# Kernel optimization log

Hardware: AMD Instinct MI355X
Metric: run time of the kernel (lower is better)

## Reference

```python
import jax, jax.numpy as jnp
import numpy as np

B, N, T, F_IN = 4, 1024, 16, 32
H1, H2 = 128, 128
LH = H2 // 2          # LSTM hidden = 64
MLP_H = H2 // 4       # 32
NEG = -9e15
ALPHA = 0.2           # LeakyReLU slope


def _xavier(k, shape):
    lim = float(np.sqrt(6.0 / (shape[0] + shape[1])))
    return jax.random.uniform(k, shape, jnp.float32, -lim, lim)


def _unif(k, shape, s):
    return jax.random.uniform(k, shape, jnp.float32, -s, s)


def setup_inputs() -> dict:
    key = jax.random.key(0)
    ks = jax.random.split(key, 16)
    x = jax.random.normal(ks[0], (B, N, T, F_IN), dtype=jnp.float32)
    adj = jax.random.randint(ks[1], (B, N, N), 0, 2, dtype=jnp.int32)
    # GAT layer 1 & 2
    W1 = _xavier(ks[2], (F_IN, H1)); a1 = _xavier(ks[3], (2 * H1, 1))
    W2 = _xavier(ks[4], (H1, H2));   a2 = _xavier(ks[5], (2 * H2, 1))
    # LSTM (torch gate order i,f,g,o)
    s = 1.0 / np.sqrt(LH)
    W_ih = _unif(ks[6], (4 * LH, H2), s)
    W_hh = _unif(ks[7], (4 * LH, LH), s)
    b_ih = _unif(ks[8], (4 * LH,), s)
    b_hh = _unif(ks[9], (4 * LH,), s)
    # Output MLP: 64 -> 32 -> 1
    s1 = 1.0 / np.sqrt(LH)
    Wo1 = _unif(ks[10], (LH, MLP_H), s1); bo1 = _unif(ks[11], (MLP_H,), s1)
    s2 = 1.0 / np.sqrt(MLP_H)
    Wo2 = _unif(ks[12], (MLP_H, 1), s2);  bo2 = _unif(ks[13], (1,), s2)
    return {"x": x, "adj": adj, "W1": W1, "a1": a1, "W2": W2, "a2": a2,
            "W_ih": W_ih, "W_hh": W_hh, "b_ih": b_ih, "b_hh": b_hh,
            "Wo1": Wo1, "bo1": bo1, "Wo2": Wo2, "bo2": bo2}


def _gat(h, mask, W, a):
    # h: (B,N,Fin) -> (B,N,Fout). Decompose cat([Wh_i,Wh_j]) @ a into two rank-1 scores.
    Wh = h @ W                             # (B,N,Fout)
    Fo = W.shape[1]
    s_src = Wh @ a[:Fo, 0]                 # (B,N)
    s_dst = Wh @ a[Fo:, 0]                 # (B,N)
    e = jax.nn.leaky_relu(s_src[:, :, None] + s_dst[:, None, :], ALPHA)  # (B,N,N)
    att = jnp.where(mask, e, NEG)
    att = jax.nn.softmax(att, axis=-1)
    return jax.nn.elu(att @ Wh)            # GAT layer's own ELU (concat=True)


def reference(x, adj, W1, a1, W2, a2, W_ih, W_hh, b_ih, b_hh, Wo1, bo1, Wo2, bo2):
    mask = adj > 0                         # (B,N,N)

    def per_t(ht):                         # ht: (B,N,F_IN)
        h = jax.nn.elu(_gat(ht, mask, W1, a1))   # outer F.elu as in GNNModel.forward
        h = jax.nn.elu(_gat(h, mask, W2, a2))
        return h

    g = jax.vmap(per_t, in_axes=2, out_axes=2)(x)   # (B,N,T,H2)
    seq = g.reshape(B * N, T, H2)

    def step(carry, xt):
        h, c = carry
        gates = xt @ W_ih.T + b_ih + h @ W_hh.T + b_hh
        i, f, gg, o = jnp.split(gates, 4, axis=-1)
        c = jax.nn.sigmoid(f) * c + jax.nn.sigmoid(i) * jnp.tanh(gg)
        h = jax.nn.sigmoid(o) * jnp.tanh(c)
        return (h, c), None

    init = (jnp.zeros((B * N, LH), x.dtype), jnp.zeros((B * N, LH), x.dtype))
    (hT, _), _ = jax.lax.scan(step, init, jnp.swapaxes(seq, 0, 1))  # scan over T

    out = jax.nn.relu(hT @ Wo1 + bo1) @ Wo2 + bo2   # (B*N, 1)
    return out.reshape(B, N, 1)
```

## Files before the change

kernel.cpp:

```cpp
#include <hip/hip_runtime.h>
#include <hip/hip_bf16.h>
#include <math.h>

#define BB 4
#define NN 1024
#define TT 16
#define FIN 32
#define HH 128
#define LH 64
#define MLPH 32

typedef __attribute__((ext_vector_type(8))) short short8;
typedef __attribute__((ext_vector_type(4))) float f32x4;
typedef unsigned short u16;
typedef unsigned int u32;

union AFu { u32 u[4]; short8 s; };

__device__ __forceinline__ u16 f2b(float f) {
    union { float f; u32 u; } v; v.f = f;
    u32 u = v.u;
    return (u16)((u + 0x7FFFu + ((u >> 16) & 1u)) >> 16);
}
__device__ __forceinline__ float b2f(u16 h) {
    union { u32 u; float f; } v; v.u = ((u32)h) << 16;
    return v.f;
}
__device__ __forceinline__ float frcp(float x) {
    float r; asm("v_rcp_f32 %0, %1" : "=v"(r) : "v"(x)); return r;
}
__device__ __forceinline__ float fsig(float x) {
    return frcp(1.f + __expf(-x));
}
__device__ __forceinline__ float ftanh(float x) {
    return __builtin_fmaf(2.f, frcp(1.f + __expf(-2.f * x)), -1.f);
}
__device__ __forceinline__ void gload_lds16(const void* g, void* l) {
    __builtin_amdgcn_global_load_lds((const __attribute__((address_space(1))) unsigned int*)g,
                                     (__attribute__((address_space(3))) unsigned int*)l, 16, 0, 0);
}

__global__ __launch_bounds__(256) void k_pre(const float* __restrict__ W1, const float* __restrict__ W2,
                      const float* __restrict__ W_ih, const float* __restrict__ W_hh,
                      const float* __restrict__ b_ih, const float* __restrict__ b_hh,
                      u16* W1T, u16* W2T, u16* WihB, u16* WhhB, float* bsum) {
    int gi = blockIdx.x * 256 + threadIdx.x;
    for (int i = gi; i < 128 * 32; i += 16384) { int c = i >> 5, k = i & 31; W1T[i] = f2b(W1[k * 128 + c]); }
    for (int i = gi; i < 128 * 128; i += 16384) { int c = i >> 7, k = i & 127; W2T[i] = f2b(W2[k * 128 + c]); }
    for (int i = gi; i < 256 * 128; i += 16384) WihB[i] = f2b(W_ih[i]);
    for (int i = gi; i < 256 * 64; i += 16384) WhhB[i] = f2b(W_hh[i]);
    if (gi < 256) bsum[gi] = b_ih[gi] + b_hh[gi];
}

__global__ __launch_bounds__(256) void k_mask(const int* __restrict__ adj, u32* __restrict__ bmT) {
    int gw = (blockIdx.x * 256 + threadIdx.x) >> 6;
    int lane = threadIdx.x & 63;
    int base = gw << 4;
#pragma unroll 4
    for (int it = 0; it < 16; ++it) {
        int u = base + it;
        unsigned long long m = __ballot(adj[((size_t)u << 6) + lane] > 0);
        if (lane == 0) {
            int g = u & 15;
            int bi = u >> 4;
            int b = bi >> 10, i = bi & 1023;
            bmT[(((b << 5) + 2 * g) << 10) + i]     = (u32)m;
            bmT[(((b << 5) + 2 * g + 1) << 10) + i] = (u32)(m >> 32);
        }
    }
}


__global__ __launch_bounds__(256) void k_projA(const float* __restrict__ x, const u16* __restrict__ W1T,
                                               const float* __restrict__ a1,
                                               u16* __restrict__ WhT, float* __restrict__ ssrc,
                                               float* __restrict__ sdst) {
    __shared__ float tile[64][132];
    __shared__ float sA[256];
    int bt = blockIdx.x >> 4, i0 = (blockIdx.x & 15) << 6;
    int b = bt >> 4, t = bt & 15;
    int tid = threadIdx.x, w = tid >> 6, l = tid & 63;
    int lr = l & 15, lg = l >> 4;
    sA[tid] = a1[tid];
    int i = i0 + 16 * w + lr;
    const float* xp = x + ((size_t)((b << 10) + i) * TT + t) * FIN + 8 * lg;
    float4 x0 = *(const float4*)xp;
    float4 x1 = *(const float4*)(xp + 4);
    short8 af;
    af[0] = (short)f2b(x0.x); af[1] = (short)f2b(x0.y); af[2] = (short)f2b(x0.z); af[3] = (short)f2b(x0.w);
    af[4] = (short)f2b(x1.x); af[5] = (short)f2b(x1.y); af[6] = (short)f2b(x1.z); af[7] = (short)f2b(x1.w);
    f32x4 zz = {0.f, 0.f, 0.f, 0.f};
#pragma unroll
    for (int tc = 0; tc < 8; ++tc) {
        short8 bf = *(const short8*)(W1T + ((16 * tc + lr) << 5) + 8 * lg);
        f32x4 d = __builtin_amdgcn_mfma_f32_16x16x32_bf16(af, bf, zz, 0, 0, 0);
#pragma unroll
        for (int r = 0; r < 4; ++r) tile[16 * w + 4 * lg + r][16 * tc + lr] = d[r];
    }
    __syncthreads();
    if (tid < 128) {
        int r = tid & 63;
        const float* av = sA + ((tid < 64) ? 0 : 128);
        float s = 0.f;
#pragma unroll 4
        for (int c = 0; c < 128; ++c) s += tile[r][c] * av[c];
        ((tid < 64) ? ssrc : sdst)[(bt << 10) + i0 + r] = s;
    }
    {
        int c = tid & 127, hh2 = tid >> 7;
        u16 tmp[32];
#pragma unroll
        for (int j = 0; j < 32; ++j) tmp[j] = f2b(tile[32 * hh2 + j][c]);
        int tc = c >> 4, lr2 = c & 15;
        u16* dst = WhT + (size_t)bt * 131072 + ((i0 >> 5) + hh2) * 4096 + tc * 512 + lr2 * 8;
#pragma unroll
        for (int lg2 = 0; lg2 < 4; ++lg2) *(short8*)(dst + lg2 * 128) = *(const short8*)(tmp + 8 * lg2);
    }
}

__global__ __launch_bounds__(256) void k_projB(const u16* __restrict__ h1, const u16* __restrict__ W2T,
                                               const float* __restrict__ a2,
                                               u16* __restrict__ WhT, float* __restrict__ ssrc,
                                               float* __restrict__ sdst) {
    __shared__ float tile[64][132];
    __shared__ float sA[256];
    int bt = blockIdx.x >> 4, i0 = (blockIdx.x & 15) << 6;
    int tid = threadIdx.x, w = tid >> 6, l = tid & 63;
    int lr = l & 15, lg = l >> 4;
    sA[tid] = a2[tid];
    const u16* ap = h1 + (size_t)bt * 131072 + ((i0 >> 4) + w) * 2048 + l * 8;
    f32x4 acc[8];
#pragma unroll
    for (int tc = 0; tc < 8; ++tc) acc[tc] = (f32x4){0.f, 0.f, 0.f, 0.f};
#pragma unroll
    for (int ch = 0; ch < 4; ++ch) {
        short8 af = *(const short8*)(ap + ch * 512);
#pragma unroll
        for (int tc = 0; tc < 8; ++tc) {
            short8 bf = *(const short8*)(W2T + ((16 * tc + lr) << 7) + 32 * ch + 8 * lg);
            acc[tc] = __builtin_amdgcn_mfma_f32_16x16x32_bf16(af, bf, acc[tc], 0, 0, 0);
        }
    }
#pragma unroll
    for (int tc = 0; tc < 8; ++tc)
#pragma unroll
        for (int r = 0; r < 4; ++r) tile[16 * w + 4 * lg + r][16 * tc + lr] = acc[tc][r];
    __syncthreads();
    if (tid < 128) {
        int r = tid & 63;
        const float* av = sA + ((tid < 64) ? 0 : 128);
        float s = 0.f;
#pragma unroll 4
        for (int c = 0; c < 128; ++c) s += tile[r][c] * av[c];
        ((tid < 64) ? ssrc : sdst)[(bt << 10) + i0 + r] = s;
    }
    {
        int c = tid & 127, hh2 = tid >> 7;
        u16 tmp[32];
#pragma unroll
        for (int j = 0; j < 32; ++j) tmp[j] = f2b(tile[32 * hh2 + j][c]);
        int tc = c >> 4, lr2 = c & 15;
        u16* dst = WhT + (size_t)bt * 131072 + ((i0 >> 5) + hh2) * 4096 + tc * 512 + lr2 * 8;
#pragma unroll
        for (int lg2 = 0; lg2 < 4; ++lg2) *(short8*)(dst + lg2 * 128) = *(const short8*)(tmp + 8 * lg2);
    }
}

#define ATTN_PROLOGUE                                                                \
    __shared__ __align__(16) u16 Bbuf[2][8192];                                      \
    __shared__ __align__(16) float Ej[1024];                                         \
    __shared__ __align__(16) float Fj[1024];                                         \
    int bt = blockIdx.x >> 2, i0b = (blockIdx.x & 3) << 8;                           \
    int b = bt >> 4;                                                                 \
    int tid = threadIdx.x, wv = tid >> 6, l = tid & 63;                              \
    int lr = l & 15, lg = l >> 4;                                                    \
    const u16* wbase = WhT + (size_t)bt * 131072;                                    \
    gload_lds16(wbase + (wv << 10) + l * 8,       &Bbuf[0][(wv << 10)]);             \
    gload_lds16(wbase + (wv << 10) + 512 + l * 8, &Bbuf[0][(wv << 10) + 512]);       \
    for (int k = tid; k < 1024; k += 512) {                                          \
        float sdv = sdst[(bt << 10) + k];                                            \
        Ej[k] = __expf(sdv);                                                         \
        Fj[k] = __expf(0.2f * sdv);                                                  \
    }                                                                                \
    int rb = i0b + (wv << 5);                                                        \
    const u32* mbase = bmT + ((size_t)b << 15);                                      \
    u32 mw0 = mbase[rb + lr];                                                        \
    u32 mw1 = mbase[rb + 16 + lr];                                                   \
    u32 mw2 = mbase[1024 + rb + lr];                                                 \
    u32 mw3 = mbase[1024 + rb + 16 + lr];                                            \
    float si0 = ssrc[(bt << 10) + rb + lr];                                          \
    float si1 = ssrc[(bt << 10) + rb + 16 + lr];                                     \
    float Ei0 = __expf(si0), Fi0 = __expf(0.2f * si0);                               \
    float Ei1 = __expf(si1), Fi1 = __expf(0.2f * si1);                               \
    f32x4 acc[2][8];                                                                 \
    _Pragma("unroll")                                                                \
    for (int rt = 0; rt < 2; ++rt)                                                   \
        _Pragma("unroll")                                                            \
        for (int tc = 0; tc < 8; ++tc) acc[rt][tc] = (f32x4){0.f, 0.f, 0.f, 0.f};    \
    f32x4 accd[2];                                                                   \
    accd[0] = (f32x4){0.f, 0.f, 0.f, 0.f};                                           \
    accd[1] = (f32x4){0.f, 0.f, 0.f, 0.f};                                           \
    short8 bone;                                                                     \
    _Pragma("unroll")                                                                \
    for (int e = 0; e < 8; ++e) bone[e] = (short)0x3F80;                             \
    __syncthreads();

#define PHALF(AF, EI, FI, WW)                                                        \
    {                                                                                \
        u32 byt = ((WW) >> (lg << 3)) & 0xFFu;                                       \
        float pA[8] = {fmaxf((EI) * e0.x, (FI) * f0.x), fmaxf((EI) * e0.y, (FI) * f0.y), \
                       fmaxf((EI) * e0.z, (FI) * f0.z), fmaxf((EI) * e0.w, (FI) * f0.w), \
                       fmaxf((EI) * e1.x, (FI) * f1.x), fmaxf((EI) * e1.y, (FI) * f1.y), \
                       fmaxf((EI) * e1.z, (FI) * f1.z), fmaxf((EI) * e1.w, (FI) * f1.w)}; \
        _Pragma("unroll")                                                            \
        for (int q = 0; q < 4; ++q) {                                                \
            u32 m0 = (u32)(-(int)((byt >> (2 * q)) & 1u));                           \
            u32 m1 = (u32)(-(int)((byt >> (2 * q + 1)) & 1u));                       \
            float p0 = __uint_as_float(__float_as_uint(pA[2 * q]) & m0);             \
            float p1 = __uint_as_float(__float_as_uint(pA[2 * q + 1]) & m1);         \
            asm("v_cvt_pk_bf16_f32 %0, %1, %2" : "=v"(AF.u[q]) : "v"(p0), "v"(p1));  \
        }                                                                            \
    }

#define COMPUTE(JC, CUR, JCL, W0, W1)                                                \
    {                                                                                \
        const float* ejp = Ej + ((JC) << 5) + (lg << 3);                             \
        const float* fjp = Fj + ((JC) << 5) + (lg << 3);                             \
        float4 e0 = *(const float4*)ejp, e1 = *(const float4*)(ejp + 4);             \
        float4 f0 = *(const float4*)fjp, f1 = *(const float4*)(fjp + 4);             \
        AFu af0, af1;                                                                \
        PHALF(af0, Ei0, Fi0, W0)                                                     \
        PHALF(af1, Ei1, Fi1, W1)                                                     \
        _Pragma("unroll")                                                            \
        for (int tc = 0; tc < 8; ++tc) {                                             \
            short8 bfr = *(const short8*)(&Bbuf[CUR][(JCL) * 4096 + tc * 512 + l * 8]); \
            acc[0][tc] = __builtin_amdgcn_mfma_f32_16x16x32_bf16(af0.s, bfr, acc[0][tc], 0, 0, 0); \
            acc[1][tc] = __builtin_amdgcn_mfma_f32_16x16x32_bf16(af1.s, bfr, acc[1][tc], 0, 0, 0); \
        }                                                                            \
        accd[0] = __builtin_amdgcn_mfma_f32_16x16x32_bf16(af0.s, bone, accd[0], 0, 0, 0); \
        accd[1] = __builtin_amdgcn_mfma_f32_16x16x32_bf16(af1.s, bone, accd[1], 0, 0, 0); \
    }

#define ATTN_MAIN_LOOP                                                               \
    for (int c = 0; c < 16; ++c) {                                                   \
        int cur = c & 1;                                                             \
        if (c < 15) {                                                                \
            gload_lds16(wbase + (c + 1) * 8192 + (wv << 10) + l * 8,       &Bbuf[cur ^ 1][(wv << 10)]);       \
            gload_lds16(wbase + (c + 1) * 8192 + (wv << 10) + 512 + l * 8, &Bbuf[cur ^ 1][(wv << 10) + 512]); \
        }                                                                            \
        u32 nw0 = 0, nw1 = 0, nw2 = 0, nw3 = 0;                                      \
        if (c < 15) {                                                                \
            const u32* mp = mbase + ((2 * c + 2) << 10);                             \
            nw0 = mp[rb + lr];        nw1 = mp[rb + 16 + lr];                        \
            nw2 = mp[1024 + rb + lr]; nw3 = mp[1024 + rb + 16 + lr];                 \
        }                                                                            \
        COMPUTE(2 * c,     cur, 0, mw0, mw1)                                         \
        COMPUTE(2 * c + 1, cur, 1, mw2, mw3)                                         \
        mw0 = nw0; mw1 = nw1; mw2 = nw2; mw3 = nw3;                                  \
        __syncthreads();                                                             \
    }

__global__ __launch_bounds__(512) void k_attnH(const u16* __restrict__ WhT, const float* __restrict__ ssrc,
                                               const float* __restrict__ sdst, const u32* __restrict__ bmT,
                                               u16* __restrict__ hout) {
    ATTN_PROLOGUE
    ATTN_MAIN_LOOP

    char* hb = (char*)(&Bbuf[0][0]) + ((wv & 3) << 13);
    for (int pass = 0; pass < 2; ++pass) {
        if ((wv >> 2) == pass) {
#pragma unroll
            for (int rt = 0; rt < 2; ++rt) {
                float inv[4];
#pragma unroll
                for (int r = 0; r < 4; ++r) inv[r] = 1.f / accd[rt][r];
#pragma unroll
                for (int tc = 0; tc < 8; ++tc)
#pragma unroll
                    for (int r = 0; r < 4; ++r) {
                        float v = acc[rt][tc][r] * inv[r];
                        v = v > 0.f ? v : (__expf(v) - 1.f);
                        v = v > 0.f ? v : (__expf(v) - 1.f);
                        int row = (rt << 4) + (lg << 2) + r;
                        int col = (tc << 4) + lr;
                        *(u16*)(hb + (row << 8) + ((col << 1) ^ ((row & 7) << 4))) = f2b(v);
                    }
            }
            asm volatile("s_waitcnt lgkmcnt(0)" ::: "memory");
            __builtin_amdgcn_sched_barrier(0);
            int rtile0 = rb >> 4;
            u16* dstb = hout + (size_t)bt * 131072;
#pragma unroll
            for (int rt = 0; rt < 2; ++rt)
#pragma unroll
                for (int ch = 0; ch < 4; ++ch) {
                    int row = (rt << 4) + lr;
                    int colb = (ch << 5) + (lg << 3);
                    short8 v = *(const short8*)(hb + (row << 8) + ((colb << 1) ^ ((row & 7) << 4)));
                    *(short8*)(dstb + (size_t)(rtile0 + rt) * 2048 + ch * 512 + l * 8) = v;
                }
        }
        __syncthreads();
    }
}

__global__ __launch_bounds__(512, 2) void k_attnG(const u16* __restrict__ WhT, const float* __restrict__ ssrc,
                                                  const float* __restrict__ sdst, const u32* __restrict__ bmT,
                                                  const u16* __restrict__ WihB, const float* __restrict__ bsum,
                                                  u16* __restrict__ Gx) {
    ATTN_PROLOGUE
    ATTN_MAIN_LOOP

    int t = bt & 15;
    char* hb = (char*)(&Bbuf[0][0]) + (wv << 12);

#define EPI_STORE(RT)                                                                 \
    {                                                                                 \
        float inv[4];                                                                 \
        _Pragma("unroll")                                                             \
        for (int r = 0; r < 4; ++r) inv[r] = 1.f / accd[RT][r];                       \
        _Pragma("unroll")                                                             \
        for (int tc = 0; tc < 8; ++tc)                                                \
            _Pragma("unroll")                                                         \
            for (int r = 0; r < 4; ++r) {                                             \
                float v = acc[RT][tc][r] * inv[r];                                    \
                v = v > 0.f ? v : (__expf(v) - 1.f);                                  \
                v = v > 0.f ? v : (__expf(v) - 1.f);                                  \
                int row = (lg << 2) + r;                                              \
                int col = (tc << 4) + lr;                                             \
                *(u16*)(hb + (row << 8) + ((col << 1) ^ ((row & 7) << 4))) = f2b(v);  \
            }                                                                         \
        asm volatile("s_waitcnt lgkmcnt(0)" ::: "memory");                            \
        __builtin_amdgcn_sched_barrier(0);                                            \
    }

#define EPI_OUT_GX(RT)                                                                \
    {                                                                                 \
        int node = i0b + (wv << 5) + ((RT) << 4);                                     \
        int grpx = (b << 6) + (node >> 4);                                            \
        u16* gdst = Gx + (size_t)t * 1048576 + (size_t)grpx * 4096 + l * 8;           \
        _Pragma("unroll")                                                             \
        for (int half = 0; half < 2; ++half) {                                        \
            f32x4 accg[8];                                                            \
            _Pragma("unroll")                                                         \
            for (int tq = 0; tq < 8; ++tq) accg[tq] = (f32x4){0.f, 0.f, 0.f, 0.f};    \
            _Pragma("unroll")                                                         \
            for (int ch = 0; ch < 4; ++ch) {                                          \
                short8 af2 = *(const short8*)(hb + (lr << 8) + (((ch << 6) + (lg << 4)) ^ ((lr & 7) << 4))); \
                _Pragma("unroll")                                                     \
                for (int tq = 0; tq < 8; ++tq) {                                      \
                    int tc = (half << 3) + tq;                                        \
                    short8 bf = *(const short8*)(WihB + ((16 * tc + lr) << 7) + (ch << 5) + 8 * lg); \
                    accg[tq] = __builtin_amdgcn_mfma_f32_16x16x32_bf16(af2, bf, accg[tq], 0, 0, 0); \
                }                                                                     \
            }                                                                         \
            _Pragma("unroll")                                                         \
            for (int qq = 0; qq < 4; ++qq) {                                          \
                int tc0 = (half << 3) + 2 * qq;                                       \
                short8 v;                                                             \
                _Pragma("unroll")                                                     \
                for (int r = 0; r < 4; ++r) {                                         \
                    v[r]     = (short)f2b(accg[2 * qq][r]     + bsum[(tc0 << 4) + lr]); \
                    v[4 + r] = (short)f2b(accg[2 * qq + 1][r] + bsum[((tc0 + 1) << 4) + lr]); \
                }                                                                     \
                *(short8*)(gdst + ((half << 2) + qq) * 512) = v;                      \
            }                                                                         \
        }                                                                             \
    }

    EPI_STORE(0)
    EPI_OUT_GX(0)
    asm volatile("s_waitcnt lgkmcnt(0)" ::: "memory");
    __builtin_amdgcn_sched_barrier(0);
    EPI_STORE(1)
    EPI_OUT_GX(1)

#undef EPI_STORE
#undef EPI_OUT_GX
}

#undef ATTN_PROLOGUE
#undef ATTN_MAIN_LOOP
#undef PHALF
#undef COMPUTE

__global__ __launch_bounds__(256, 1) void k_lstm(const u16* __restrict__ Gx, const u16* __restrict__ WhhB,
                                                 const float* __restrict__ Wo1, const float* __restrict__ bo1,
                                                 const float* __restrict__ Wo2, const float* __restrict__ bo2,
                                                 float* __restrict__ out) {
    __shared__ u16 hls[16 * 72];
    __shared__ float hf[16 * 65];
    __shared__ float wo1[64 * 32];
    __shared__ float wo2[32];
    int grp = blockIdx.x;
    int m0 = grp << 4;
    int tid = threadIdx.x, wv = tid >> 6, l = tid & 63;
    int lr = l & 15, lg = l >> 4;
    for (int k = tid; k < 64 * 32; k += 256) wo1[k] = Wo1[k];
    if (tid < 32) wo2[tid] = Wo2[tid];
    for (int k = tid; k < 16 * 72; k += 256) hls[k] = 0;
    short8 bh[4][2];
#pragma unroll
    for (int tq = 0; tq < 4; ++tq)
#pragma unroll
        for (int ch = 0; ch < 2; ++ch)
            bh[tq][ch] = *(const short8*)(WhhB + ((16 * (wv + 4 * tq) + lr) << 6) + 32 * ch + 8 * lg);
    float cst[4], hreg[4];
#pragma unroll
    for (int r = 0; r < 4; ++r) { cst[r] = 0.f; hreg[r] = 0.f; }
    int sub = wv & 1;
    const u16* gp = Gx + ((size_t)grp << 12) + ((size_t)(wv >> 1) << 9) + l * 8;
    short8 gx0[4], gx1[4];
#pragma unroll
    for (int tq = 0; tq < 4; ++tq) gx0[tq] = *(const short8*)(gp + tq * 1024);
    __syncthreads();
#pragma unroll
    for (int t = 0; t < TT; ++t) {
        if (t < 15) {
#pragma unroll
            for (int tq = 0; tq < 4; ++tq) {
                short8 v = *(const short8*)(gp + (size_t)(t + 1) * 1048576 + tq * 1024);
                if (t & 1) gx0[tq] = v; else gx1[tq] = v;
            }
        }
        f32x4 acc[4];
#pragma unroll
        for (int tq = 0; tq < 4; ++tq) {
            short8 v = (t & 1) ? gx1[tq] : gx0[tq];
#pragma unroll
            for (int r = 0; r < 4; ++r)
                acc[tq][r] = b2f((u16)v[(sub << 2) + r]);
        }
#pragma unroll
        for (int ch = 0; ch < 2; ++ch) {
            short8 af = *(const short8*)(hls + lr * 72 + 32 * ch + 8 * lg);
#pragma unroll
            for (int tq = 0; tq < 4; ++tq)
                acc[tq] = __builtin_amdgcn_mfma_f32_16x16x32_bf16(af, bh[tq][ch], acc[tq], 0, 0, 0);
        }
#pragma unroll
        for (int r = 0; r < 4; ++r) {
            float iv = fsig(acc[0][r]);
            float fv = fsig(acc[1][r]);
            float gv = ftanh(acc[2][r]);
            float ov = fsig(acc[3][r]);
            float cn = __builtin_fmaf(fv, cst[r], iv * gv);
            cst[r] = cn;
            hreg[r] = ov * ftanh(cn);
        }
        __syncthreads();
#pragma unroll
        for (int r = 0; r < 4; ++r)
            hls[(4 * lg + r) * 72 + 16 * wv + lr] = f2b(hreg[r]);
        __syncthreads();
    }
#pragma unroll
    for (int r = 0; r < 4; ++r)
        hf[(4 * lg + r) * 65 + 16 * wv + lr] = hreg[r];
    __syncthreads();
    if (wv == 0) {
        int r = lr, p = lg;
        float hid[8];
#pragma unroll
        for (int q = 0; q < 8; ++q) hid[q] = bo1[8 * p + q];
        for (int j = 0; j < 64; ++j) {
            float hv = hf[r * 65 + j];
#pragma unroll
            for (int q = 0; q < 8; ++q) hid[q] += hv * wo1[j * 32 + 8 * p + q];
        }
        float po = 0.f;
#pragma unroll
        for (int q = 0; q < 8; ++q) po += fmaxf(hid[q], 0.f) * wo2[8 * p + q];
        po += __shfl_xor(po, 16);
        po += __shfl_xor(po, 32);
        if (p == 0) out[m0 + r] = po + bo2[0];
    }
}

extern "C" void kernel_launch(void* const* d_in, const int* in_sizes, int n_in,
                              void* d_out, int out_size, void* d_ws, size_t ws_size,
                              hipStream_t stream) {
    const float* x    = (const float*)d_in[0];
    const int*   adj  = (const int*)d_in[1];
    const float* W1   = (const float*)d_in[2];
    const float* a1   = (const float*)d_in[3];
    const float* W2   = (const float*)d_in[4];
    const float* a2   = (const float*)d_in[5];
    const float* W_ih = (const float*)d_in[6];
    const float* W_hh = (const float*)d_in[7];
    const float* b_ih = (const float*)d_in[8];
    const float* b_hh = (const float*)d_in[9];
    const float* Wo1  = (const float*)d_in[10];
    const float* bo1  = (const float*)d_in[11];
    const float* Wo2  = (const float*)d_in[12];
    const float* bo2  = (const float*)d_in[13];
    float* out = (float*)d_out;

    char* w = (char*)d_ws;
    const size_t SLOT = (size_t)8388608 * sizeof(u16);
    u16* A  = (u16*)w;
    u16* Bf = (u16*)(w + SLOT);
    u16* C  = (u16*)(w + 2 * SLOT);
    char* sm = w + 3 * SLOT;
    float* s1s = (float*)sm;
    float* s1d = s1s + 65536;
    float* s2s = s1d + 65536;
    float* s2d = s2s + 65536;
    u32* BM  = (u32*)(s2d + 65536);
    u16* W1T = (u16*)(BM + 131072);
    u16* W2T = W1T + 4096;
    u16* WihB = W2T + 16384;
    u16* WhhB = WihB + 32768;
    float* BS = (float*)(WhhB + 16384);
    u16* Gx = Bf;

    k_pre<<<64, 256, 0, stream>>>(W1, W2, W_ih, W_hh, b_ih, b_hh, W1T, W2T, WihB, WhhB, BS);
    k_mask<<<1024, 256, 0, stream>>>(adj, BM);
    k_projA<<<1024, 256, 0, stream>>>(x, W1T, a1, A, s1s, s1d);
    k_attnH<<<256, 512, 0, stream>>>(A, s1s, s1d, BM, Bf);
    k_projB<<<1024, 256, 0, stream>>>(Bf, W2T, a2, C, s2s, s2d);
    k_attnG<<<256, 512, 0, stream>>>(C, s2s, s2d, BM, WihB, BS, Gx);
    k_lstm<<<256, 256, 0, stream>>>(Gx, WhhB, Wo1, bo1, Wo2, bo2, out);
}
```

Baseline: 166.7 us.

## Fuse layer-2 GAT projection and score computation into layer-1 attention epilogue

Removes the separate k_projB kernel and performs the layer-2 W2 projection plus src/dst attention scores inside k_attnH's epilogue. Each wave writes its ELU'd tile to LDS, runs MFMA against W2T and stores the bf16 Wh2 tile directly, reducing the scores with shuffles. This drops a kernel launch and the global round-trip of the hidden activations, but adds register pressure (launch bounds now 512,2) and W2T global reads in every block.

```diff
diff --git a/kernel.cpp b/kernel.cpp
--- a/kernel.cpp
+++ b/kernel.cpp
@@ -11,6 +11,7 @@
 #define MLPH 32
 
 typedef __attribute__((ext_vector_type(8))) short short8;
+typedef __attribute__((ext_vector_type(4))) short short4v;
 typedef __attribute__((ext_vector_type(4))) float f32x4;
 typedef unsigned short u16;
 typedef unsigned int u32;
@@ -97,54 +98,6 @@
 #pragma unroll
         for (int r = 0; r < 4; ++r) tile[16 * w + 4 * lg + r][16 * tc + lr] = d[r];
     }
-    __syncthreads();
-    if (tid < 128) {
-        int r = tid & 63;
-        const float* av = sA + ((tid < 64) ? 0 : 128);
-        float s = 0.f;
-#pragma unroll 4
-        for (int c = 0; c < 128; ++c) s += tile[r][c] * av[c];
-        ((tid < 64) ? ssrc : sdst)[(bt << 10) + i0 + r] = s;
-    }
-    {
-        int c = tid & 127, hh2 = tid >> 7;
-        u16 tmp[32];
-#pragma unroll
-        for (int j = 0; j < 32; ++j) tmp[j] = f2b(tile[32 * hh2 + j][c]);
-        int tc = c >> 4, lr2 = c & 15;
-        u16* dst = WhT + (size_t)bt * 131072 + ((i0 >> 5) + hh2) * 4096 + tc * 512 + lr2 * 8;
-#pragma unroll
-        for (int lg2 = 0; lg2 < 4; ++lg2) *(short8*)(dst + lg2 * 128) = *(const short8*)(tmp + 8 * lg2);
-    }
-}
-
-__global__ __launch_bounds__(256) void k_projB(const u16* __restrict__ h1, const u16* __restrict__ W2T,
-                                               const float* __restrict__ a2,
-                                               u16* __restrict__ WhT, float* __restrict__ ssrc,
-                                               float* __restrict__ sdst) {
-    __shared__ float tile[64][132];
-    __shared__ float sA[256];
-    int bt = blockIdx.x >> 4, i0 = (blockIdx.x & 15) << 6;
-    int tid = threadIdx.x, w = tid >> 6, l = tid & 63;
-    int lr = l & 15, lg = l >> 4;
-    sA[tid] = a2[tid];
-    const u16* ap = h1 + (size_t)bt * 131072 + ((i0 >> 4) + w) * 2048 + l * 8;
-    f32x4 acc[8];
-#pragma unroll
-    for (int tc = 0; tc < 8; ++tc) acc[tc] = (f32x4){0.f, 0.f, 0.f, 0.f};
-#pragma unroll
-    for (int ch = 0; ch < 4; ++ch) {
-        short8 af = *(const short8*)(ap + ch * 512);
-#pragma unroll
-        for (int tc = 0; tc < 8; ++tc) {
-            short8 bf = *(const short8*)(W2T + ((16 * tc + lr) << 7) + 32 * ch + 8 * lg);
-            acc[tc] = __builtin_amdgcn_mfma_f32_16x16x32_bf16(af, bf, acc[tc], 0, 0, 0);
-        }
-    }
-#pragma unroll
-    for (int tc = 0; tc < 8; ++tc)
-#pragma unroll
-        for (int r = 0; r < 4; ++r) tile[16 * w + 4 * lg + r][16 * tc + lr] = acc[tc][r];
     __syncthreads();
     if (tid < 128) {
         int r = tid & 63;
@@ -260,48 +213,103 @@
         __syncthreads();                                                             \
     }
 
-__global__ __launch_bounds__(512) void k_attnH(const u16* __restrict__ WhT, const float* __restrict__ ssrc,
-                                               const float* __restrict__ sdst, const u32* __restrict__ bmT,
-                                               u16* __restrict__ hout) {
+__global__ __launch_bounds__(512, 2) void k_attnH(const u16* __restrict__ WhT, const float* __restrict__ ssrc,
+                                                  const float* __restrict__ sdst, const u32* __restrict__ bmT,
+                                                  const u16* __restrict__ W2T, const float* __restrict__ a2,
+                                                  u16* __restrict__ Wh2, float* __restrict__ s2s,
+                                                  float* __restrict__ s2d) {
     ATTN_PROLOGUE
     ATTN_MAIN_LOOP
 
-    char* hb = (char*)(&Bbuf[0][0]) + ((wv & 3) << 13);
-    for (int pass = 0; pass < 2; ++pass) {
-        if ((wv >> 2) == pass) {
-#pragma unroll
-            for (int rt = 0; rt < 2; ++rt) {
-                float inv[4];
-#pragma unroll
-                for (int r = 0; r < 4; ++r) inv[r] = 1.f / accd[rt][r];
-#pragma unroll
-                for (int tc = 0; tc < 8; ++tc)
-#pragma unroll
-                    for (int r = 0; r < 4; ++r) {
-                        float v = acc[rt][tc][r] * inv[r];
-                        v = v > 0.f ? v : (__expf(v) - 1.f);
-                        v = v > 0.f ? v : (__expf(v) - 1.f);
-                        int row = (rt << 4) + (lg << 2) + r;
-                        int col = (tc << 4) + lr;
-                        *(u16*)(hb + (row << 8) + ((col << 1) ^ ((row & 7) << 4))) = f2b(v);
-                    }
-            }
-            asm volatile("s_waitcnt lgkmcnt(0)" ::: "memory");
-            __builtin_amdgcn_sched_barrier(0);
-            int rtile0 = rb >> 4;
-            u16* dstb = hout + (size_t)bt * 131072;
-#pragma unroll
-            for (int rt = 0; rt < 2; ++rt)
-#pragma unroll
-                for (int ch = 0; ch < 4; ++ch) {
-                    int row = (rt << 4) + lr;
-                    int colb = (ch << 5) + (lg << 3);
-                    short8 v = *(const short8*)(hb + (row << 8) + ((colb << 1) ^ ((row & 7) << 4)));
-                    *(short8*)(dstb + (size_t)(rtile0 + rt) * 2048 + ch * 512 + l * 8) = v;
-                }
-        }
-        __syncthreads();
-    }
+    char* hb = (char*)(&Bbuf[0][0]) + (wv << 12);
+
+#define EPI_STORE(RT)                                                                 \
+    {                                                                                 \
+        float inv[4];                                                                 \
+        _Pragma("unroll")                                                             \
+        for (int r = 0; r < 4; ++r) inv[r] = 1.f / accd[RT][r];                       \
+        _Pragma("unroll")                                                             \
+        for (int tc = 0; tc < 8; ++tc)                                                \
+            _Pragma("unroll")                                                         \
+            for (int r = 0; r < 4; ++r) {                                             \
+                float v = acc[RT][tc][r] * inv[r];                                    \
+                v = v > 0.f ? v : (__expf(v) - 1.f);                                  \
+                v = v > 0.f ? v : (__expf(v) - 1.f);                                  \
+                int row = (lg << 2) + r;                                              \
+                int col = (tc << 4) + lr;                                             \
+                *(u16*)(hb + (row << 8) + ((col << 1) ^ ((row & 7) << 4))) = f2b(v);  \
+            }                                                                         \
+        asm volatile("s_waitcnt lgkmcnt(0)" ::: "memory");                            \
+        __builtin_amdgcn_sched_barrier(0);                                            \
+    }
+
+#define EPI_PROJB(RT)                                                                 \
+    {                                                                                 \
+        float ps[4], pd[4];                                                           \
+        _Pragma("unroll")                                                             \
+        for (int r = 0; r < 4; ++r) { ps[r] = 0.f; pd[r] = 0.f; }                     \
+        int grow = i0b + (wv << 5) + ((RT) << 4);                                     \
+        int jc = grow >> 5;                                                           \
+        u16* wout = Wh2 + (size_t)bt * 131072 + jc * 4096;                            \
+        int lg2 = 2 * (RT) + (lg >> 1);                                               \
+        _Pragma("unroll")                                                             \
+        for (int half = 0; half < 2; ++half) {                                        \
+            f32x4 accg[4];                                                            \
+            _Pragma("unroll")                                                         \
+            for (int tq = 0; tq < 4; ++tq) accg[tq] = (f32x4){0.f, 0.f, 0.f, 0.f};    \
+            _Pragma("unroll")                                                         \
+            for (int ch = 0; ch < 4; ++ch) {                                          \
+                short8 af2 = *(const short8*)(hb + (lr << 8) + (((ch << 6) + (lg << 4)) ^ ((lr & 7) << 4))); \
+                _Pragma("unroll")                                                     \
+                for (int tq = 0; tq < 4; ++tq) {                                      \
+                    int tc2 = (half << 2) + tq;                                       \
+                    short8 bf = *(const short8*)(W2T + ((16 * tc2 + lr) << 7) + (ch << 5) + 8 * lg); \
+                    accg[tq] = __builtin_amdgcn_mfma_f32_16x16x32_bf16(af2, bf, accg[tq], 0, 0, 0); \
+                }                                                                     \
+            }                                                                         \
+            _Pragma("unroll")                                                         \
+            for (int tq = 0; tq < 4; ++tq) {                                          \
+                int tc2 = (half << 2) + tq;                                           \
+                float a2sv = a2[16 * tc2 + lr];                                       \
+                float a2dv = a2[128 + 16 * tc2 + lr];                                 \
+                short4v w4;                                                           \
+                _Pragma("unroll")                                                     \
+                for (int r = 0; r < 4; ++r) {                                         \
+                    float wval = accg[tq][r];                                         \
+                    ps[r] = __builtin_fmaf(wval, a2sv, ps[r]);                        \
+                    pd[r] = __builtin_fmaf(wval, a2dv, pd[r]);                        \
+                    w4[r] = (short)f2b(wval);                                         \
+                }                                                                     \
+                *(short4v*)(wout + tc2 * 512 + lg2 * 128 + lr * 8 + (lg & 1) * 4) = w4; \
+            }                                                                         \
+        }                                                                             \
+        _Pragma("unroll")                                                             \
+        for (int r = 0; r < 4; ++r) {                                                 \
+            _Pragma("unroll")                                                         \
+            for (int o = 1; o < 16; o <<= 1) {                                        \
+                ps[r] += __shfl_xor(ps[r], o);                                        \
+                pd[r] += __shfl_xor(pd[r], o);                                        \
+            }                                                                         \
+        }                                                                             \
+        if (lr == 0) {                                                                \
+            _Pragma("unroll")                                                         \
+            for (int r = 0; r < 4; ++r) {                                             \
+                int row = grow + 4 * lg + r;                                          \
+                s2s[(bt << 10) + row] = ps[r];                                        \
+                s2d[(bt << 10) + row] = pd[r];                                        \
+            }                                                                         \
+        }                                                                             \
+    }
+
+    EPI_STORE(0)
+    EPI_PROJB(0)
+    asm volatile("s_waitcnt lgkmcnt(0)" ::: "memory");
+    __builtin_amdgcn_sched_barrier(0);
+    EPI_STORE(1)
+    EPI_PROJB(1)
+
+#undef EPI_STORE
+#undef EPI_PROJB
 }
 
 __global__ __launch_bounds__(512, 2) void k_attnG(const u16* __restrict__ WhT, const float* __restrict__ ssrc,
@@ -517,8 +525,7 @@
     k_pre<<<64, 256, 0, stream>>>(W1, W2, W_ih, W_hh, b_ih, b_hh, W1T, W2T, WihB, WhhB, BS);
     k_mask<<<1024, 256, 0, stream>>>(adj, BM);
     k_projA<<<1024, 256, 0, stream>>>(x, W1T, a1, A, s1s, s1d);
-    k_attnH<<<256, 512, 0, stream>>>(A, s1s, s1d, BM, Bf);
-    k_projB<<<1024, 256, 0, stream>>>(Bf, W2T, a2, C, s2s, s2d);
+    k_attnH<<<256, 512, 0, stream>>>(A, s1s, s1d, BM, W2T, a2, C, s2s, s2d);
     k_attnG<<<256, 512, 0, stream>>>(C, s2s, s2d, BM, WihB, BS, Gx);
     k_lstm<<<256, 256, 0, stream>>>(Gx, WhhB, Wo1, bo1, Wo2, bo2, out);
 }
```

After: 157.1 us. 1.06x faster.

## Fuse layer-2 projection into attention epilogue and use 1024-thread attention blocks

Applied to the files above, without the earlier changes.

The separate k_projB kernel is removed. Its bf16 MFMA projection by W2, along with the a2 source and destination score reductions, now runs in the k_attnH epilogue directly from a per-wave LDS tile, so layer-1 output no longer round-trips through global memory. Both attention kernels move from 512 to 1024 threads per block, with each wave owning 16 rows instead of 32. This halves per-wave accumulator registers but raises LDS use with a 64KB Hls buffer, and it forces one block per CU.

```diff
diff --git a/kernel.cpp b/kernel.cpp
--- a/kernel.cpp
+++ b/kernel.cpp
@@ -11,6 +11,7 @@
 #define MLPH 32
 
 typedef __attribute__((ext_vector_type(8))) short short8;
+typedef __attribute__((ext_vector_type(4))) short short4v;
 typedef __attribute__((ext_vector_type(4))) float f32x4;
 typedef unsigned short u16;
 typedef unsigned int u32;
@@ -118,100 +119,44 @@
     }
 }
 
-__global__ __launch_bounds__(256) void k_projB(const u16* __restrict__ h1, const u16* __restrict__ W2T,
-                                               const float* __restrict__ a2,
-                                               u16* __restrict__ WhT, float* __restrict__ ssrc,
-                                               float* __restrict__ sdst) {
-    __shared__ float tile[64][132];
-    __shared__ float sA[256];
-    int bt = blockIdx.x >> 4, i0 = (blockIdx.x & 15) << 6;
-    int tid = threadIdx.x, w = tid >> 6, l = tid & 63;
-    int lr = l & 15, lg = l >> 4;
-    sA[tid] = a2[tid];
-    const u16* ap = h1 + (size_t)bt * 131072 + ((i0 >> 4) + w) * 2048 + l * 8;
-    f32x4 acc[8];
-#pragma unroll
-    for (int tc = 0; tc < 8; ++tc) acc[tc] = (f32x4){0.f, 0.f, 0.f, 0.f};
-#pragma unroll
-    for (int ch = 0; ch < 4; ++ch) {
-        short8 af = *(const short8*)(ap + ch * 512);
-#pragma unroll
-        for (int tc = 0; tc < 8; ++tc) {
-            short8 bf = *(const short8*)(W2T + ((16 * tc + lr) << 7) + 32 * ch + 8 * lg);
-            acc[tc] = __builtin_amdgcn_mfma_f32_16x16x32_bf16(af, bf, acc[tc], 0, 0, 0);
-        }
-    }
-#pragma unroll
-    for (int tc = 0; tc < 8; ++tc)
-#pragma unroll
-        for (int r = 0; r < 4; ++r) tile[16 * w + 4 * lg + r][16 * tc + lr] = acc[tc][r];
-    __syncthreads();
-    if (tid < 128) {
-        int r = tid & 63;
-        const float* av = sA + ((tid < 64) ? 0 : 128);
-        float s = 0.f;
-#pragma unroll 4
-        for (int c = 0; c < 128; ++c) s += tile[r][c] * av[c];
-        ((tid < 64) ? ssrc : sdst)[(bt << 10) + i0 + r] = s;
-    }
-    {
-        int c = tid & 127, hh2 = tid >> 7;
-        u16 tmp[32];
-#pragma unroll
-        for (int j = 0; j < 32; ++j) tmp[j] = f2b(tile[32 * hh2 + j][c]);
-        int tc = c >> 4, lr2 = c & 15;
-        u16* dst = WhT + (size_t)bt * 131072 + ((i0 >> 5) + hh2) * 4096 + tc * 512 + lr2 * 8;
-#pragma unroll
-        for (int lg2 = 0; lg2 < 4; ++lg2) *(short8*)(dst + lg2 * 128) = *(const short8*)(tmp + 8 * lg2);
-    }
-}
-
 #define ATTN_PROLOGUE                                                                \
     __shared__ __align__(16) u16 Bbuf[2][8192];                                      \
     __shared__ __align__(16) float Ej[1024];                                         \
     __shared__ __align__(16) float Fj[1024];                                         \
+    __shared__ __align__(16) u16 Hls[16][2048];                                      \
     int bt = blockIdx.x >> 2, i0b = (blockIdx.x & 3) << 8;                           \
     int b = bt >> 4;                                                                 \
     int tid = threadIdx.x, wv = tid >> 6, l = tid & 63;                              \
     int lr = l & 15, lg = l >> 4;                                                    \
     const u16* wbase = WhT + (size_t)bt * 131072;                                    \
-    gload_lds16(wbase + (wv << 10) + l * 8,       &Bbuf[0][(wv << 10)]);             \
-    gload_lds16(wbase + (wv << 10) + 512 + l * 8, &Bbuf[0][(wv << 10) + 512]);       \
-    for (int k = tid; k < 1024; k += 512) {                                          \
-        float sdv = sdst[(bt << 10) + k];                                            \
-        Ej[k] = __expf(sdv);                                                         \
-        Fj[k] = __expf(0.2f * sdv);                                                  \
+    gload_lds16(wbase + (wv << 9) + l * 8, &Bbuf[0][(wv << 9)]);                     \
+    {                                                                                \
+        float sdv = sdst[(bt << 10) + tid];                                          \
+        Ej[tid] = __expf(sdv);                                                       \
+        Fj[tid] = __expf(0.2f * sdv);                                                \
     }                                                                                \
-    int rb = i0b + (wv << 5);                                                        \
+    int rb = i0b + (wv << 4);                                                        \
     const u32* mbase = bmT + ((size_t)b << 15);                                      \
     u32 mw0 = mbase[rb + lr];                                                        \
-    u32 mw1 = mbase[rb + 16 + lr];                                                   \
-    u32 mw2 = mbase[1024 + rb + lr];                                                 \
-    u32 mw3 = mbase[1024 + rb + 16 + lr];                                            \
+    u32 mw1 = mbase[1024 + rb + lr];                                                 \
     float si0 = ssrc[(bt << 10) + rb + lr];                                          \
-    float si1 = ssrc[(bt << 10) + rb + 16 + lr];                                     \
     float Ei0 = __expf(si0), Fi0 = __expf(0.2f * si0);                               \
-    float Ei1 = __expf(si1), Fi1 = __expf(0.2f * si1);                               \
-    f32x4 acc[2][8];                                                                 \
+    f32x4 acc[8];                                                                    \
     _Pragma("unroll")                                                                \
-    for (int rt = 0; rt < 2; ++rt)                                                   \
-        _Pragma("unroll")                                                            \
-        for (int tc = 0; tc < 8; ++tc) acc[rt][tc] = (f32x4){0.f, 0.f, 0.f, 0.f};    \
-    f32x4 accd[2];                                                                   \
-    accd[0] = (f32x4){0.f, 0.f, 0.f, 0.f};                                           \
-    accd[1] = (f32x4){0.f, 0.f, 0.f, 0.f};                                           \
+    for (int tc = 0; tc < 8; ++tc) acc[tc] = (f32x4){0.f, 0.f, 0.f, 0.f};            \
+    f32x4 accd = (f32x4){0.f, 0.f, 0.f, 0.f};                                        \
     short8 bone;                                                                     \
     _Pragma("unroll")                                                                \
     for (int e = 0; e < 8; ++e) bone[e] = (short)0x3F80;                             \
     __syncthreads();
 
-#define PHALF(AF, EI, FI, WW)                                                        \
+#define PHALF(AF, WW)                                                                \
     {                                                                                \
         u32 byt = ((WW) >> (lg << 3)) & 0xFFu;                                       \
-        float pA[8] = {fmaxf((EI) * e0.x, (FI) * f0.x), fmaxf((EI) * e0.y, (FI) * f0.y), \
-                       fmaxf((EI) * e0.z, (FI) * f0.z), fmaxf((EI) * e0.w, (FI) * f0.w), \
-                       fmaxf((EI) * e1.x, (FI) * f1.x), fmaxf((EI) * e1.y, (FI) * f1.y), \
-                       fmaxf((EI) * e1.z, (FI) * f1.z), fmaxf((EI) * e1.w, (FI) * f1.w)}; \
+        float pA[8] = {fmaxf(Ei0 * e0.x, Fi0 * f0.x), fmaxf(Ei0 * e0.y, Fi0 * f0.y), \
+                       fmaxf(Ei0 * e0.z, Fi0 * f0.z), fmaxf(Ei0 * e0.w, Fi0 * f0.w), \
+                       fmaxf(Ei0 * e1.x, Fi0 * f1.x), fmaxf(Ei0 * e1.y, Fi0 * f1.y), \
+                       fmaxf(Ei0 * e1.z, Fi0 * f1.z), fmaxf(Ei0 * e1.w, Fi0 * f1.w)}; \
         _Pragma("unroll")                                                            \
         for (int q = 0; q < 4; ++q) {                                                \
             u32 m0 = (u32)(-(int)((byt >> (2 * q)) & 1u));                           \
@@ -222,167 +167,172 @@
         }                                                                            \
     }
 
-#define COMPUTE(JC, CUR, JCL, W0, W1)                                                \
+#define COMPUTE(JC, CUR, JCL, W0)                                                    \
     {                                                                                \
         const float* ejp = Ej + ((JC) << 5) + (lg << 3);                             \
         const float* fjp = Fj + ((JC) << 5) + (lg << 3);                             \
         float4 e0 = *(const float4*)ejp, e1 = *(const float4*)(ejp + 4);             \
         float4 f0 = *(const float4*)fjp, f1 = *(const float4*)(fjp + 4);             \
-        AFu af0, af1;                                                                \
-        PHALF(af0, Ei0, Fi0, W0)                                                     \
-        PHALF(af1, Ei1, Fi1, W1)                                                     \
+        AFu af0;                                                                     \
+        PHALF(af0, W0)                                                               \
         _Pragma("unroll")                                                            \
         for (int tc = 0; tc < 8; ++tc) {                                             \
             short8 bfr = *(const short8*)(&Bbuf[CUR][(JCL) * 4096 + tc * 512 + l * 8]); \
-            acc[0][tc] = __builtin_amdgcn_mfma_f32_16x16x32_bf16(af0.s, bfr, acc[0][tc], 0, 0, 0); \
-            acc[1][tc] = __builtin_amdgcn_mfma_f32_16x16x32_bf16(af1.s, bfr, acc[1][tc], 0, 0, 0); \
+            acc[tc] = __builtin_amdgcn_mfma_f32_16x16x32_bf16(af0.s, bfr, acc[tc], 0, 0, 0); \
         }                                                                            \
-        accd[0] = __builtin_amdgcn_mfma_f32_16x16x32_bf16(af0.s, bone, accd[0], 0, 0, 0); \
-        accd[1] = __builtin_amdgcn_mfma_f32_16x16x32_bf16(af1.s, bone, accd[1], 0, 0, 0); \
+        accd = __builtin_amdgcn_mfma_f32_16x16x32_bf16(af0.s, bone, accd, 0, 0, 0);  \
     }
 
 #define ATTN_MAIN_LOOP                                                               \
     for (int c = 0; c < 16; ++c) {                                                   \
         int cur = c & 1;                                                             \
-        if (c < 15) {                                                                \
-            gload_lds16(wbase + (c + 1) * 8192 + (wv << 10) + l * 8,       &Bbuf[cur ^ 1][(wv << 10)]);       \
-            gload_lds16(wbase + (c + 1) * 8192 + (wv << 10) + 512 + l * 8, &Bbuf[cur ^ 1][(wv << 10) + 512]); \
-        }                                                                            \
-        u32 nw0 = 0, nw1 = 0, nw2 = 0, nw3 = 0;                                      \
+        if (c < 15)                                                                  \
+            gload_lds16(wbase + (c + 1) * 8192 + (wv << 9) + l * 8, &Bbuf[cur ^ 1][(wv << 9)]); \
+        u32 nw0 = 0, nw1 = 0;                                                        \
         if (c < 15) {                                                                \
             const u32* mp = mbase + ((2 * c + 2) << 10);                             \
-            nw0 = mp[rb + lr];        nw1 = mp[rb + 16 + lr];                        \
-            nw2 = mp[1024 + rb + lr]; nw3 = mp[1024 + rb + 16 + lr];                 \
+            nw0 = mp[rb + lr];                                                       \
+            nw1 = mp[1024 + rb + lr];                                                \
         }                                                                            \
-        COMPUTE(2 * c,     cur, 0, mw0, mw1)                                         \
-        COMPUTE(2 * c + 1, cur, 1, mw2, mw3)                                         \
-        mw0 = nw0; mw1 = nw1; mw2 = nw2; mw3 = nw3;                                  \
+        COMPUTE(2 * c,     cur, 0, mw0)                                              \
+        COMPUTE(2 * c + 1, cur, 1, mw1)                                              \
+        mw0 = nw0; mw1 = nw1;                                                        \
         __syncthreads();                                                             \
     }
 
-__global__ __launch_bounds__(512) void k_attnH(const u16* __restrict__ WhT, const float* __restrict__ ssrc,
-                                               const float* __restrict__ sdst, const u32* __restrict__ bmT,
-                                               u16* __restrict__ hout) {
+#define EPI_STORE_H                                                                  \
+    {                                                                                \
+        float inv[4];                                                                \
+        _Pragma("unroll")                                                            \
+        for (int r = 0; r < 4; ++r) inv[r] = 1.f / accd[r];                          \
+        _Pragma("unroll")                                                            \
+        for (int tc = 0; tc < 8; ++tc)                                               \
+            _Pragma("unroll")                                                        \
+            for (int r = 0; r < 4; ++r) {                                            \
+                float v = acc[tc][r] * inv[r];                                       \
+                v = v > 0.f ? v : (__expf(v) - 1.f);                                 \
+                v = v > 0.f ? v : (__expf(v) - 1.f);                                 \
+                int row = (lg << 2) + r;                                             \
+                int col = (tc << 4) + lr;                                            \
+                hb[(row << 7) + (col ^ ((row & 7) << 3))] = f2b(v);                  \
+            }                                                                        \
+    }
+
+__global__ __launch_bounds__(1024, 1) void k_attnH(const u16* __restrict__ WhT, const float* __restrict__ ssrc,
+                                                   const float* __restrict__ sdst, const u32* __restrict__ bmT,
+                                                   const u16* __restrict__ W2T, const float* __restrict__ a2,
+                                                   u16* __restrict__ Wh2, float* __restrict__ s2s,
+                                                   float* __restrict__ s2d) {
     ATTN_PROLOGUE
     ATTN_MAIN_LOOP
 
-    char* hb = (char*)(&Bbuf[0][0]) + ((wv & 3) << 13);
-    for (int pass = 0; pass < 2; ++pass) {
-        if ((wv >> 2) == pass) {
-#pragma unroll
-            for (int rt = 0; rt < 2; ++rt) {
-                float inv[4];
-#pragma unroll
-                for (int r = 0; r < 4; ++r) inv[r] = 1.f / accd[rt][r];
-#pragma unroll
-                for (int tc = 0; tc < 8; ++tc)
-#pragma unroll
-                    for (int r = 0; r < 4; ++r) {
-                        float v = acc[rt][tc][r] * inv[r];
-                        v = v > 0.f ? v : (__expf(v) - 1.f);
-                        v = v > 0.f ? v : (__expf(v) - 1.f);
-                        int row = (rt << 4) + (lg << 2) + r;
-                        int col = (tc << 4) + lr;
-                        *(u16*)(hb + (row << 8) + ((col << 1) ^ ((row & 7) << 4))) = f2b(v);
-                    }
-            }
-            asm volatile("s_waitcnt lgkmcnt(0)" ::: "memory");
-            __builtin_amdgcn_sched_barrier(0);
-            int rtile0 = rb >> 4;
-            u16* dstb = hout + (size_t)bt * 131072;
-#pragma unroll
-            for (int rt = 0; rt < 2; ++rt)
-#pragma unroll
-                for (int ch = 0; ch < 4; ++ch) {
-                    int row = (rt << 4) + lr;
-                    int colb = (ch << 5) + (lg << 3);
-                    short8 v = *(const short8*)(hb + (row << 8) + ((colb << 1) ^ ((row & 7) << 4)));
-                    *(short8*)(dstb + (size_t)(rtile0 + rt) * 2048 + ch * 512 + l * 8) = v;
+    u16* hb = &Hls[wv][0];
+    EPI_STORE_H
+
+    {
+        float ps[4], pd[4];
+#pragma unroll
+        for (int r = 0; r < 4; ++r) { ps[r] = 0.f; pd[r] = 0.f; }
+        int jc2 = rb >> 5;
+        int lgf = ((wv & 1) << 1) + (lg >> 1);
+        u16* wout = Wh2 + (size_t)bt * 131072 + jc2 * 4096;
+#pragma unroll
+        for (int half = 0; half < 2; ++half) {
+            f32x4 accg[4];
+#pragma unroll
+            for (int tq = 0; tq < 4; ++tq) accg[tq] = (f32x4){0.f, 0.f, 0.f, 0.f};
+#pragma unroll
+            for (int ch = 0; ch < 4; ++ch) {
+                short8 af2 = *(const short8*)(hb + (lr << 7) + (((ch << 5) + (lg << 3)) ^ ((lr & 7) << 3)));
+#pragma unroll
+                for (int tq = 0; tq < 4; ++tq) {
+                    int tc2 = (half << 2) + tq;
+                    short8 bf = *(const short8*)(W2T + ((16 * tc2 + lr) << 7) + (ch << 5) + 8 * lg);
+                    accg[tq] = __builtin_amdgcn_mfma_f32_16x16x32_bf16(af2, bf, accg[tq], 0, 0, 0);
                 }
-        }
-        __syncthreads();
-    }
-}
-
-__global__ __launch_bounds__(512, 2) void k_attnG(const u16* __restrict__ WhT, const float* __restrict__ ssrc,
-                                                  const float* __restrict__ sdst, const u32* __restrict__ bmT,
-                                                  const u16* __restrict__ WihB, const float* __restrict__ bsum,
-                                                  u16* __restrict__ Gx) {
+            }
+#pragma unroll
+            for (int tq = 0; tq < 4; ++tq) {
+                int tc2 = (half << 2) + tq;
+                float a2sv = a2[16 * tc2 + lr];
+                float a2dv = a2[128 + 16 * tc2 + lr];
+                short4v w4;
+#pragma unroll
+                for (int r = 0; r < 4; ++r) {
+                    float wval = accg[tq][r];
+                    ps[r] = __builtin_fmaf(wval, a2sv, ps[r]);
+                    pd[r] = __builtin_fmaf(wval, a2dv, pd[r]);
+                    w4[r] = (short)f2b(wval);
+                }
+                *(short4v*)(wout + tc2 * 512 + lgf * 128 + lr * 8 + (lg & 1) * 4) = w4;
+            }
+        }
+#pragma unroll
+        for (int r = 0; r < 4; ++r) {
+#pragma unroll
+            for (int o = 1; o < 16; o <<= 1) {
+                ps[r] += __shfl_xor(ps[r], o);
+                pd[r] += __shfl_xor(pd[r], o);
+            }
+        }
+        if (lr == 0) {
+#pragma unroll
+            for (int r = 0; r < 4; ++r) {
+                int row = rb + 4 * lg + r;
+                s2s[(bt << 10) + row] = ps[r];
+                s2d[(bt << 10) + row] = pd[r];
+            }
+        }
+    }
+}
+
+__global__ __launch_bounds__(1024, 1) void k_attnG(const u16* __restrict__ WhT, const float* __restrict__ ssrc,
+                                                   const float* __restrict__ sdst, const u32* __restrict__ bmT,
+                                                   const u16* __restrict__ WihB, const float* __restrict__ bsum,
+                                                   u16* __restrict__ Gx) {
     ATTN_PROLOGUE
     ATTN_MAIN_LOOP
 
+    u16* hb = &Hls[wv][0];
+    EPI_STORE_H
+
     int t = bt & 15;
-    char* hb = (char*)(&Bbuf[0][0]) + (wv << 12);
-
-#define EPI_STORE(RT)                                                                 \
-    {                                                                                 \
-        float inv[4];                                                                 \
-        _Pragma("unroll")                                                             \
-        for (int r = 0; r < 4; ++r) inv[r] = 1.f / accd[RT][r];                       \
-        _Pragma("unroll")                                                             \
-        for (int tc = 0; tc < 8; ++tc)                                                \
-            _Pragma("unroll")                                                         \
-            for (int r = 0; r < 4; ++r) {                                             \
-                float v = acc[RT][tc][r] * inv[r];                                    \
-                v = v > 0.f ? v : (__expf(v) - 1.f);                                  \
-                v = v > 0.f ? v : (__expf(v) - 1.f);                                  \
-                int row = (lg << 2) + r;                                              \
-                int col = (tc << 4) + lr;                                             \
-                *(u16*)(hb + (row << 8) + ((col << 1) ^ ((row & 7) << 4))) = f2b(v);  \
-            }                                                                         \
-        asm volatile("s_waitcnt lgkmcnt(0)" ::: "memory");                            \
-        __builtin_amdgcn_sched_barrier(0);                                            \
-    }
-
-#define EPI_OUT_GX(RT)                                                                \
-    {                                                                                 \
-        int node = i0b + (wv << 5) + ((RT) << 4);                                     \
-        int grpx = (b << 6) + (node >> 4);                                            \
-        u16* gdst = Gx + (size_t)t * 1048576 + (size_t)grpx * 4096 + l * 8;           \
-        _Pragma("unroll")                                                             \
-        for (int half = 0; half < 2; ++half) {                                        \
-            f32x4 accg[8];                                                            \
-            _Pragma("unroll")                                                         \
-            for (int tq = 0; tq < 8; ++tq) accg[tq] = (f32x4){0.f, 0.f, 0.f, 0.f};    \
-            _Pragma("unroll")                                                         \
-            for (int ch = 0; ch < 4; ++ch) {                                          \
-                short8 af2 = *(const short8*)(hb + (lr << 8) + (((ch << 6) + (lg << 4)) ^ ((lr & 7) << 4))); \
-                _Pragma("unroll")                                                     \
-                for (int tq = 0; tq < 8; ++tq) {                                      \
-                    int tc = (half << 3) + tq;                                        \
-                    short8 bf = *(const short8*)(WihB + ((16 * tc + lr) << 7) + (ch << 5) + 8 * lg); \
-                    accg[tq] = __builtin_amdgcn_mfma_f32_16x16x32_bf16(af2, bf, accg[tq], 0, 0, 0); \
-                }                                                                     \
-            }                                                                         \
-            _Pragma("unroll")                                                         \
-            for (int qq = 0; qq < 4; ++qq) {                                          \
-                int tc0 = (half << 3) + 2 * qq;                                       \
-                short8 v;                                                             \
-                _Pragma("unroll")                                                     \
-                for (int r = 0; r < 4; ++r) {                                         \
-                    v[r]     = (short)f2b(accg[2 * qq][r]     + bsum[(tc0 << 4) + lr]); \
-                    v[4 + r] = (short)f2b(accg[2 * qq + 1][r] + bsum[((tc0 + 1) << 4) + lr]); \
-                }                                                                     \
-                *(short8*)(gdst + ((half << 2) + qq) * 512) = v;                      \
-            }                                                                         \
-        }                                                                             \
-    }
-
-    EPI_STORE(0)
-    EPI_OUT_GX(0)
-    asm volatile("s_waitcnt lgkmcnt(0)" ::: "memory");
-    __builtin_amdgcn_sched_barrier(0);
-    EPI_STORE(1)
-    EPI_OUT_GX(1)
-
-#undef EPI_STORE
-#undef EPI_OUT_GX
+    int grpx = (b << 6) + (rb >> 4);
+    u16* gdst = Gx + (size_t)t * 1048576 + (size_t)grpx * 4096 + l * 8;
+#pragma unroll
+    for (int half = 0; half < 2; ++half) {
+        f32x4 accg[8];
+#pragma unroll
+        for (int tq = 0; tq < 8; ++tq) accg[tq] = (f32x4){0.f, 0.f, 0.f, 0.f};
+#pragma unroll
+        for (int ch = 0; ch < 4; ++ch) {
+            short8 af2 = *(const short8*)(hb + (lr << 7) + (((ch << 5) + (lg << 3)) ^ ((lr & 7) << 3)));
+#pragma unroll
+            for (int tq = 0; tq < 8; ++tq) {
+                int tc = (half << 3) + tq;
+                short8 bf = *(const short8*)(WihB + ((16 * tc + lr) << 7) + (ch << 5) + 8 * lg);
+                accg[tq] = __builtin_amdgcn_mfma_f32_16x16x32_bf16(af2, bf, accg[tq], 0, 0, 0);
+            }
+        }
+#pragma unroll
+        for (int qq = 0; qq < 4; ++qq) {
+            int tc0 = (half << 3) + 2 * qq;
+            short8 v;
+#pragma unroll
+            for (int r = 0; r < 4; ++r) {
+                v[r]     = (short)f2b(accg[2 * qq][r]     + bsum[(tc0 << 4) + lr]);
+                v[4 + r] = (short)f2b(accg[2 * qq + 1][r] + bsum[((tc0 + 1) << 4) + lr]);
+            }
+            *(short8*)(gdst + ((half << 2) + qq) * 512) = v;
+        }
+    }
 }
 
 #undef ATTN_PROLOGUE
 #undef ATTN_MAIN_LOOP
 #undef PHALF
 #undef COMPUTE
+#undef EPI_STORE_H
 
 __global__ __launch_bounds__(256, 1) void k_lstm(const u16* __restrict__ Gx, const u16* __restrict__ WhhB,
                                                  const float* __restrict__ Wo1, const float* __restrict__ bo1,
@@ -517,8 +467,7 @@
     k_pre<<<64, 256, 0, stream>>>(W1, W2, W_ih, W_hh, b_ih, b_hh, W1T, W2T, WihB, WhhB, BS);
     k_mask<<<1024, 256, 0, stream>>>(adj, BM);
     k_projA<<<1024, 256, 0, stream>>>(x, W1T, a1, A, s1s, s1d);
-    k_attnH<<<256, 512, 0, stream>>>(A, s1s, s1d, BM, Bf);
-    k_projB<<<1024, 256, 0, stream>>>(Bf, W2T, a2, C, s2s, s2d);
-    k_attnG<<<256, 512, 0, stream>>>(C, s2s, s2d, BM, WihB, BS, Gx);
+    k_attnH<<<256, 1024, 0, stream>>>(A, s1s, s1d, BM, W2T, a2, C, s2s, s2d);
+    k_attnG<<<256, 1024, 0, stream>>>(C, s2s, s2d, BM, WihB, BS, Gx);
     k_lstm<<<256, 256, 0, stream>>>(Gx, WhhB, Wo1, bo1, Wo2, bo2, out);
 }
```

After: 151.4 us. -9.2%, faster.
